# Kernel optimization log

Hardware: AMD Instinct MI355X
Metric: run time of the kernel (lower is better)

Reference implementation:

```python
import jax, jax.numpy as jnp
import numpy as np

T, B, C, HS, RD = 32, 32, 128, 512, 3  # timesteps, batch, state_channels, hidden_size, recurse_depth
HW = 7


def setup_inputs() -> dict:
    key = jax.random.key(0)
    ks = jax.random.split(key, 6)
    x = jax.random.normal(ks[0], (T * B, C, HW, HW), jnp.float32)
    hxs = jax.random.normal(ks[1], (B, 2 * C, HW, HW), jnp.float32)
    masks = jax.random.uniform(ks[2], (T * B,), jnp.float32)
    # ConvLSTMCell: conv over concat(x, h) [2C in] -> 4C gate channels, 3x3, bias
    Wconv = jax.random.normal(ks[3], (4 * C, 2 * C, 3, 3), jnp.float32) * 0.02
    bconv = jnp.zeros((4 * C,), jnp.float32)
    # flat_lin: Linear(C*7*7 -> hidden_size), torch layout [out, in]
    Wlin = jax.random.normal(ks[4], (HS, C * HW * HW), jnp.float32) * 0.02
    blin = jnp.zeros((HS,), jnp.float32)
    return {"x": x, "hxs": hxs, "masks": masks, "Wconv": Wconv, "bconv": bconv, "Wlin": Wlin, "blin": blin}


def reference(x, hxs, masks, Wconv, bconv, Wlin, blin):
    xs = x.reshape(T, B, C, HW, HW)
    ms = masks.reshape(T, B)
    h0, c0 = hxs[:, :C], hxs[:, C:]

    def conv_gates(inp):  # [B, 2C, 7, 7] -> [B, 4C, 7, 7]
        y = jax.lax.conv_general_dilated(
            inp, Wconv, window_strides=(1, 1), padding="SAME",
            dimension_numbers=("NCHW", "OIHW", "NCHW"))
        return y + bconv[None, :, None, None]

    def step(carry, inp):
        h, c = carry
        x_t, m_t = inp
        m = m_t[:, None, None, None]
        h = h * m
        c = c * m
        for _ in range(RD):  # recurse_depth inner unroll (sequential dependency)
            g = conv_gates(jnp.concatenate([x_t, h], axis=1))
            cc_i, cc_f, cc_o, cc_g = jnp.split(g, 4, axis=1)
            i = jax.nn.sigmoid(cc_i)
            f = jax.nn.sigmoid(cc_f)
            o = jax.nn.sigmoid(cc_o)
            gg = jnp.tanh(cc_g)
            c = f * c + i * gg
            h = o * jnp.tanh(c)
        out = jax.nn.relu(c.reshape(B, -1) @ Wlin.T + blin)  # flat_lin applied to c
        return (h, c), out

    (hT, cT), outs = jax.lax.scan(step, (h0, c0), (xs, ms))
    return outs.reshape(T * B, HS), jnp.concatenate([hT, cT], axis=1)
```

## Files before the change

### kernel.cpp

```cpp
#include <hip/hip_runtime.h>
#include <hip/hip_bf16.h>
#include <stdint.h>

#define T_  32
#define B_  32
#define C_  128
#define HS_ 512
#define HW_ 7
#define S_  49
#define CS_  (C_*S_)
#define ICS_ (2*C_*S_)
#define KH_  1152
#define KL_  6272
#define M_   1568
#define N_   512

typedef __attribute__((ext_vector_type(8))) short short8;
typedef __attribute__((ext_vector_type(4))) float f32x4;
typedef __hip_bfloat16 bf16;

union bfbits { bf16 b; short s; };

__device__ __forceinline__ void gl16(const void* g, void* l) {
    __builtin_amdgcn_global_load_lds((const __attribute__((address_space(1))) void*)g,
                                     (__attribute__((address_space(3))) void*)l, 16, 0, 0);
}

__device__ __forceinline__ float sigm_f(float v) { return 1.0f / (1.0f + __expf(-v)); }
__device__ __forceinline__ float tanh_f(float v) { return 1.0f - 2.0f / (__expf(2.0f * v) + 1.0f); }

__global__ __launch_bounds__(256, 2) void k_fgemm(
    const bf16* __restrict__ xTt, const bf16* __restrict__ hT,
    bf16* __restrict__ hTN,
    const bf16* __restrict__ WxP, const bf16* __restrict__ WhP,
    const float* __restrict__ bconv,
    float* __restrict__ Gx, float* __restrict__ cbuf,
    const float* __restrict__ mask_c, const float* __restrict__ mask_a,
    bf16* __restrict__ chist_t, const bf16* __restrict__ zb, int mode0)
{
    __shared__ bf16 sA[2][32 * 64];
    __shared__ bf16 sB[2][64 * 64];
    __shared__ float gld[32][68];

    const int tid = threadIdx.x, lane = tid & 63, w = tid >> 6;
    const int m0 = blockIdx.x * 32, n0 = blockIdx.y * 64;

    const int ar   = tid >> 3;
    const int akq  = tid & 7;
    const int am_  = m0 + ar;
    const int ab   = am_ / S_;
    const int as_  = am_ % S_;
    const int ayy  = as_ / HW_, axx = as_ % HW_;
    const int aswz = ((akq ^ (ar & 7)) << 3);

    const int br0 = tid >> 3;
    const int br1 = (256 + tid) >> 3;
    const int bswz0 = (((tid & 7) ^ (br0 & 7)) << 3);
    const int bswz1 = (((tid & 7) ^ (br1 & 7)) << 3);

    const int NS = mode0 ? 36 : 18;

    f32x4 accX[2], accH[2];
    if (mode0) {
        int np = n0 + w * 16 + (lane & 15);
        float bv = bconv[((np & 3) << 7) + (np >> 2)];
        f32x4 b4 = {bv, bv, bv, bv};
        accX[0] = b4; accX[1] = b4;
        f32x4 z4 = {0.f, 0.f, 0.f, 0.f};
        accH[0] = z4; accH[1] = z4;
    } else {
#pragma unroll
        for (int fm = 0; fm < 2; ++fm) {
            int row = m0 + fm * 16 + ((lane >> 4) << 2);
            int col = n0 + w * 16 + (lane & 15);
#pragma unroll
            for (int j = 0; j < 4; ++j) accH[fm][j] = Gx[(size_t)(row + j) * N_ + col];
        }
    }

    auto stageFor = [&](int st, bf16* lA, bf16* lB) {
        int xphase = (mode0 && st < 18);
        int stl = (mode0 && st >= 18) ? st - 18 : st;
        int kid = stl >> 1, koff = (stl & 1) << 6;
        int ky = kid / 3, kx = kid - ky * 3;
        int y2 = ayy + ky - 1, x2 = axx + kx - 1;
        const bf16* Asrc = xphase ? xTt : hT;
        const bf16* rbase;
        if ((unsigned)y2 < (unsigned)HW_ && (unsigned)x2 < (unsigned)HW_)
            rbase = Asrc + (((size_t)ab * S_ + y2 * HW_ + x2) << 7) + koff;
        else
            rbase = zb;
        gl16(rbase + aswz, lA + w * 512);
        const bf16* Wsrc = xphase ? WxP : WhP;
        gl16(Wsrc + (size_t)(n0 + br0) * KH_ + stl * 64 + bswz0, lB + w * 512);
        gl16(Wsrc + (size_t)(n0 + br1) * KH_ + stl * 64 + bswz1, lB + 2048 + w * 512);
    };

    auto computeFrom = [&](const bf16* sAc, const bf16* sBc, f32x4 (&acc)[2]) {
        short8 af[2][2], bq[2];
#pragma unroll
        for (int kh = 0; kh < 2; ++kh) {
#pragma unroll
            for (int fm = 0; fm < 2; ++fm) {
                int r = fm * 16 + (lane & 15);
                int kc = kh * 4 + (lane >> 4);
                af[fm][kh] = *(const short8*)(sAc + r * 64 + ((kc ^ (r & 7)) << 3));
            }
            { int r = w * 16 + (lane & 15);
              int kc = kh * 4 + (lane >> 4);
              bq[kh] = *(const short8*)(sBc + r * 64 + ((kc ^ (r & 7)) << 3)); }
        }
#pragma unroll
        for (int kh = 0; kh < 2; ++kh)
#pragma unroll
            for (int fm = 0; fm < 2; ++fm)
                acc[fm] = __builtin_amdgcn_mfma_f32_16x16x32_bf16(af[fm][kh], bq[kh], acc[fm], 0, 0, 0);
    };

    stageFor(0, sA[0], sB[0]);
    __syncthreads();

#pragma unroll 1
    for (int st = 0; st < NS; st += 2) {
        if (st + 1 < NS) stageFor(st + 1, sA[1], sB[1]);
        if (mode0 && st < 18) computeFrom(sA[0], sB[0], accX);
        else                  computeFrom(sA[0], sB[0], accH);
        __syncthreads();
        if (st + 2 < NS) stageFor(st + 2, sA[0], sB[0]);
        if (mode0 && st + 1 < 18) computeFrom(sA[1], sB[1], accX);
        else                      computeFrom(sA[1], sB[1], accH);
        __syncthreads();
    }

    if (mode0) {
#pragma unroll
        for (int fm = 0; fm < 2; ++fm) {
            int row = m0 + fm * 16 + ((lane >> 4) << 2);
            int col = n0 + w * 16 + (lane & 15);
#pragma unroll
            for (int j = 0; j < 4; ++j) {
                Gx[(size_t)(row + j) * N_ + col] = accX[fm][j];
                accH[fm][j] += accX[fm][j];
            }
        }
    }

#pragma unroll
    for (int fm = 0; fm < 2; ++fm) {
        int row = fm * 16 + ((lane >> 4) << 2);
        int col = w * 16 + (lane & 15);
#pragma unroll
        for (int j = 0; j < 4; ++j) gld[row + j][col] = accH[fm][j];
    }
    __syncthreads();

#pragma unroll
    for (int q = 0; q < 2; ++q) {
        int e = tid * 2 + q;
        int row = e >> 4, cc = e & 15;
        int m = m0 + row;
        int b = m / S_, s = m % S_;
        int cg = (n0 >> 2) + cc;
        float g0 = gld[row][cc * 4 + 0], g1 = gld[row][cc * 4 + 1];
        float g2 = gld[row][cc * 4 + 2], g3 = gld[row][cc * 4 + 3];
        float ig = sigm_f(g0);
        float fg = sigm_f(g1);
        float og = sigm_f(g2);
        float gg = tanh_f(g3);
        size_t ci = (((size_t)b * S_ + s) << 7) + cg;
        float co = cbuf[ci];
        if (mask_c) co *= mask_c[b];
        float cn = fg * co + ig * gg;
        cbuf[ci] = cn;
        float hn = og * tanh_f(cn);
        float am = mask_a ? mask_a[b] : 1.f;
        hTN[ci] = __float2bfloat16(hn * am);
        if (chist_t) chist_t[(size_t)b * KL_ + s * C_ + cg] = __float2bfloat16(cn);
    }
}

__device__ __forceinline__ void stage64(
    const bf16* __restrict__ srcA, int strideA, int m0, int kA0,
    const bf16* __restrict__ srcB, int strideB, int n0, int kB0,
    bf16* ldsA, bf16* ldsB, int w, int lane)
{
#pragma unroll
    for (int p = 0; p < 2; ++p) {
        int slot = p * 256 + w * 64 + lane;
        int r  = slot >> 3;
        int kq = slot & 7;
        int kqs = (kq ^ (r & 7)) << 3;
        gl16(srcA + (size_t)(m0 + r) * strideA + kA0 + kqs, ldsA + p * 2048 + w * 512);
        gl16(srcB + (size_t)(n0 + r) * strideB + kB0 + kqs, ldsB + p * 2048 + w * 512);
    }
}

__global__ __launch_bounds__(256, 2) void k_lingemm(
    const bf16* __restrict__ Ac, const bf16* __restrict__ Wl,
    const float* __restrict__ blin, float* __restrict__ out)
{
    __shared__ bf16 sA[2][64 * 64];
    __shared__ bf16 sB[2][64 * 64];

    const int tid = threadIdx.x, lane = tid & 63, w = tid >> 6;
    const int wr = w >> 1, wc = w & 1;
    const int m0 = blockIdx.x * 64, n0 = blockIdx.y * 64;

    f32x4 acc[2][2];
#pragma unroll
    for (int fn = 0; fn < 2; ++fn) {
        int np = n0 + wc * 32 + fn * 16 + (lane & 15);
        float bv = blin[np];
        f32x4 b4 = {bv, bv, bv, bv};
        acc[0][fn] = b4; acc[1][fn] = b4;
    }

    auto stageFor = [&](int s2, bf16* lA, bf16* lB) {
        stage64(Ac, KL_, m0, s2 * 64, Wl, KL_, n0, s2 * 64, lA, lB, w, lane);
    };
    auto computeFrom = [&](const bf16* sAc, const bf16* sBc) {
        short8 af[2][2], bq[2][2];
#pragma unroll
        for (int f = 0; f < 2; ++f)
#pragma unroll
            for (int kh = 0; kh < 2; ++kh) {
                { int r = wr * 32 + f * 16 + (lane & 15);
                  int kc = kh * 4 + (lane >> 4);
                  af[f][kh] = *(const short8*)(sAc + r * 64 + ((kc ^ (r & 7)) << 3)); }
                { int r = wc * 32 + f * 16 + (lane & 15);
                  int kc = kh * 4 + (lane >> 4);
                  bq[f][kh] = *(const short8*)(sBc + r * 64 + ((kc ^ (r & 7)) << 3)); }
            }
#pragma unroll
        for (int kh = 0; kh < 2; ++kh)
#pragma unroll
            for (int fm = 0; fm < 2; ++fm)
#pragma unroll
                for (int fn = 0; fn < 2; ++fn)
                    acc[fm][fn] = __builtin_amdgcn_mfma_f32_16x16x32_bf16(
                        af[fm][kh], bq[fn][kh], acc[fm][fn], 0, 0, 0);
    };

    stageFor(0, sA[0], sB[0]);
    __syncthreads();

#pragma unroll 1
    for (int st = 0; st < 98; st += 2) {
        if (st + 1 < 98) stageFor(st + 1, sA[1], sB[1]);
        computeFrom(sA[0], sB[0]);
        __syncthreads();
        if (st + 2 < 98) stageFor(st + 2, sA[0], sB[0]);
        computeFrom(sA[1], sB[1]);
        __syncthreads();
    }

#pragma unroll
    for (int fm = 0; fm < 2; ++fm)
#pragma unroll
        for (int fn = 0; fn < 2; ++fn) {
            int col = n0 + wc * 32 + fn * 16 + (lane & 15);
            int rb  = m0 + wr * 32 + fm * 16 + ((lane >> 4) << 2);
#pragma unroll
            for (int j = 0; j < 4; ++j)
                out[(size_t)(rb + j) * N_ + col] = fmaxf(acc[fm][fn][j], 0.f);
        }
}

__global__ __launch_bounds__(256) void k_wsplit(const float* __restrict__ Wc,
                                               bf16* __restrict__ WxP, bf16* __restrict__ WhP) {
    int idx = blockIdx.x * 256 + threadIdx.x;
    if (idx >= 512 * 288) return;
    int np = idx / 288, kq = idx % 288;
    int oc = ((np & 3) << 7) + (np >> 2);
    int kk = kq * 8;
    int half = kk >= KH_;
    int krel = kk - half * KH_;
    short8 v;
#pragma unroll
    for (int j = 0; j < 8; ++j) {
        int kr = krel + j;
        int kid = kr >> 7, ic = (kr & 127) + half * 128;
        bfbits bb; bb.b = __float2bfloat16(Wc[((size_t)oc * 256 + ic) * 9 + kid]);
        v[j] = bb.s;
    }
    bf16* dst = half ? WhP : WxP;
    *reinterpret_cast<short8*>(dst + (size_t)np * KH_ + krel) = v;
}

__global__ __launch_bounds__(256) void k_wlin2(const float* __restrict__ Wl, bf16* __restrict__ Wp) {
    int idx = blockIdx.x * 256 + threadIdx.x;
    if (idx >= 512 * 784) return;
    int np = idx / 784, kq = idx % 784;
    short8 v;
#pragma unroll
    for (int j = 0; j < 8; ++j) {
        int kp = kq * 8 + j;
        int s = kp >> 7, c = kp & 127;
        bfbits bb; bb.b = __float2bfloat16(Wl[(size_t)np * KL_ + c * S_ + s]);
        v[j] = bb.s;
    }
    *reinterpret_cast<short8*>(Wp + (size_t)np * KL_ + kq * 8) = v;
}

__global__ __launch_bounds__(256) void k_xpose(const float* __restrict__ x, bf16* __restrict__ xT) {
    int idx = blockIdx.x * 256 + threadIdx.x;
    if (idx >= 1024 * 784) return;
    int r = idx / 784;
    int rem = idx % 784;
    int s = rem / 16, c8 = (rem & 15) * 8;
    const float* sp = x + (size_t)r * CS_ + c8 * S_ + s;
    short8 v;
#pragma unroll
    for (int j = 0; j < 8; ++j) { bfbits bb; bb.b = __float2bfloat16(sp[j * S_]); v[j] = bb.s; }
    *reinterpret_cast<short8*>(xT + (((size_t)r * S_ + s) << 7) + c8) = v;
}

__global__ __launch_bounds__(256) void k_hcprep(const float* __restrict__ hxs,
                                                const float* __restrict__ mask0,
                                                bf16* __restrict__ hT, float* __restrict__ cbuf) {
    int idx = blockIdx.x * 256 + threadIdx.x;
    if (idx >= 32 * 784) return;
    int b = idx / 784;
    int rem = idx % 784;
    int s = rem / 16, c8 = (rem & 15) * 8;
    float m = mask0[b];
    const float* hp = hxs + (size_t)b * ICS_ + c8 * S_ + s;
    const float* cp = hp + CS_;
    size_t o = (((size_t)b * S_ + s) << 7) + c8;
    short8 v;
#pragma unroll
    for (int j = 0; j < 8; ++j) {
        bfbits bb; bb.b = __float2bfloat16(hp[j * S_] * m); v[j] = bb.s;
        cbuf[o + j] = cp[j * S_];
    }
    *reinterpret_cast<short8*>(hT + o) = v;
}

__global__ __launch_bounds__(256) void k_zero16(uint4* __restrict__ p, int n) {
    int i = blockIdx.x * 256 + threadIdx.x;
    if (i < n) p[i] = make_uint4(0, 0, 0, 0);
}

__global__ __launch_bounds__(256) void k_final(const bf16* __restrict__ hT, const float* __restrict__ cbuf,
                                               float* __restrict__ out) {
    int i = blockIdx.x * 256 + threadIdx.x;
    if (i >= B_ * ICS_) return;
    int b = i / ICS_, r = i % ICS_;
    int ch = r / S_, s = r % S_;
    size_t o = (((size_t)b * S_ + s) << 7);
    out[i] = (ch < C_) ? __bfloat162float(hT[o + ch]) : cbuf[o + (ch - C_)];
}

extern "C" void kernel_launch(void* const* d_in, const int* in_sizes, int n_in,
                              void* d_out, int out_size, void* d_ws, size_t ws_size,
                              hipStream_t stream) {
    (void)in_sizes; (void)n_in; (void)out_size; (void)ws_size;
    const float* x     = (const float*)d_in[0];
    const float* hxs   = (const float*)d_in[1];
    const float* masks = (const float*)d_in[2];
    const float* Wconv = (const float*)d_in[3];
    const float* bconv = (const float*)d_in[4];
    const float* Wlin  = (const float*)d_in[5];
    const float* blin  = (const float*)d_in[6];
    float* out = (float*)d_out;

    uint8_t* p = (uint8_t*)d_ws;
    bf16* WxP   = (bf16*)p;   p += (size_t)512 * KH_ * 2;
    bf16* WhP   = (bf16*)p;   p += (size_t)512 * KH_ * 2;
    bf16* Wlp   = (bf16*)p;   p += (size_t)512 * KL_ * 2;
    bf16* xT    = (bf16*)p;   p += (size_t)1024 * S_ * C_ * 2;
    bf16* hA    = (bf16*)p;   p += (size_t)B_ * S_ * C_ * 2;
    bf16* hB    = (bf16*)p;   p += (size_t)B_ * S_ * C_ * 2;
    float* cbuf = (float*)p;  p += (size_t)B_ * S_ * C_ * 4;
    float* Gx   = (float*)p;  p += (size_t)M_ * N_ * 4;
    bf16* chist = (bf16*)p;   p += (size_t)1024 * KL_ * 2;
    bf16* zb    = (bf16*)p;   p += 1024;
    bf16* hbufs[2] = {hA, hB};

    k_wsplit<<<576, 256, 0, stream>>>(Wconv, WxP, WhP);
    k_wlin2<<<1568, 256, 0, stream>>>(Wlin, Wlp);
    k_xpose<<<3136, 256, 0, stream>>>(x, xT);
    k_hcprep<<<98, 256, 0, stream>>>(hxs, masks, hA, cbuf);
    k_zero16<<<1, 256, 0, stream>>>((uint4*)zb, 64);

    int g = 0;
    for (int t = 0; t < T_; ++t) {
        const bf16* xTt = xT + (size_t)t * B_ * S_ * C_;
        for (int rd = 0; rd < 3; ++rd) {
            const float* mc = (rd == 0) ? masks + (size_t)t * B_ : nullptr;
            const float* ma = (rd == 2 && t < T_ - 1) ? masks + (size_t)(t + 1) * B_ : nullptr;
            bf16* ct = (rd == 2) ? chist + (size_t)t * B_ * KL_ : nullptr;
            k_fgemm<<<dim3(49, 8), 256, 0, stream>>>(
                (rd == 0) ? xTt : nullptr, hbufs[g & 1], hbufs[(g + 1) & 1],
                WxP, WhP, bconv, Gx, cbuf, mc, ma, ct, zb, (rd == 0) ? 1 : 0);
            ++g;
        }
    }

    k_lingemm<<<dim3(16, 8), 256, 0, stream>>>(chist, Wlp, blin, out);
    k_final<<<1568, 256, 0, stream>>>(hbufs[0], cbuf, out + (size_t)T_ * B_ * HS_);
}
```

Before: 1.714 ms.

## Enlarge recurrent conv GEMM tile to 64x64 with K=128 stages

The per-step conv-gate GEMM now uses 64x64 output tiles per block (2x2 warp layout) instead of 32x64, and both GEMMs stage 128-wide K chunks per step with a single sync per stage instead of 64-wide chunks. The aim is to halve the number of barriers and global-to-LDS staging rounds and to raise operand reuse per loaded tile. In exchange the recurrent kernel launches only 200 blocks instead of 392, which lowers parallelism across the GPU's compute units on this latency-bound sequential chain. The LDS footprint grows to 64KB, and Gx is padded so the partial last row tile stays in bounds.

```diff
diff --git a/kernel.cpp b/kernel.cpp
--- a/kernel.cpp
+++ b/kernel.cpp
@@ -13,6 +13,7 @@
 #define KH_  1152
 #define KL_  6272
 #define M_   1568
+#define MR_  1600
 #define N_   512
 
 typedef __attribute__((ext_vector_type(8))) short short8;
@@ -38,128 +39,145 @@
     const float* __restrict__ mask_c, const float* __restrict__ mask_a,
     bf16* __restrict__ chist_t, const bf16* __restrict__ zb, int mode0)
 {
-    __shared__ bf16 sA[2][32 * 64];
-    __shared__ bf16 sB[2][64 * 64];
-    __shared__ float gld[32][68];
+    __shared__ __align__(16) uint8_t smem[65536];
+    bf16* sA = (bf16*)smem;
+    bf16* sB = (bf16*)(smem + 32768);
+    float (*gld)[68] = (float(*)[68])smem;
 
     const int tid = threadIdx.x, lane = tid & 63, w = tid >> 6;
-    const int m0 = blockIdx.x * 32, n0 = blockIdx.y * 64;
-
-    const int ar   = tid >> 3;
-    const int akq  = tid & 7;
-    const int am_  = m0 + ar;
-    const int ab   = am_ / S_;
-    const int as_  = am_ % S_;
-    const int ayy  = as_ / HW_, axx = as_ % HW_;
-    const int aswz = ((akq ^ (ar & 7)) << 3);
-
-    const int br0 = tid >> 3;
-    const int br1 = (256 + tid) >> 3;
-    const int bswz0 = (((tid & 7) ^ (br0 & 7)) << 3);
-    const int bswz1 = (((tid & 7) ^ (br1 & 7)) << 3);
-
-    const int NS = mode0 ? 36 : 18;
-
-    f32x4 accX[2], accH[2];
+    const int wr = w >> 1, wc = w & 1;
+    const int m0 = blockIdx.x * 64, n0 = blockIdx.y * 64;
+
+    const int kq = tid & 15, rr = tid >> 4;
+    const int swz = ((kq ^ rr) << 3);
+    int abS[4], ay[4], ax[4]; bool rok[4];
+#pragma unroll
+    for (int q = 0; q < 4; ++q) {
+        int ra = m0 + q * 16 + rr;
+        rok[q] = ra < M_;
+        int b = ra / S_, s = ra - b * S_;
+        abS[q] = b * S_;
+        ay[q] = s / HW_; ax[q] = s - ay[q] * HW_;
+    }
+
+    const int NS = mode0 ? 18 : 9;
+
+    f32x4 accX[2][2], accH[2][2];
     if (mode0) {
-        int np = n0 + w * 16 + (lane & 15);
-        float bv = bconv[((np & 3) << 7) + (np >> 2)];
-        f32x4 b4 = {bv, bv, bv, bv};
-        accX[0] = b4; accX[1] = b4;
-        f32x4 z4 = {0.f, 0.f, 0.f, 0.f};
-        accH[0] = z4; accH[1] = z4;
+#pragma unroll
+        for (int fn = 0; fn < 2; ++fn) {
+            int np = n0 + wc * 32 + fn * 16 + (lane & 15);
+            float bv = bconv[((np & 3) << 7) + (np >> 2)];
+            f32x4 b4 = {bv, bv, bv, bv};
+            accX[0][fn] = b4; accX[1][fn] = b4;
+            f32x4 z4 = {0.f, 0.f, 0.f, 0.f};
+            accH[0][fn] = z4; accH[1][fn] = z4;
+        }
     } else {
 #pragma unroll
         for (int fm = 0; fm < 2; ++fm) {
-            int row = m0 + fm * 16 + ((lane >> 4) << 2);
-            int col = n0 + w * 16 + (lane & 15);
-#pragma unroll
-            for (int j = 0; j < 4; ++j) accH[fm][j] = Gx[(size_t)(row + j) * N_ + col];
-        }
-    }
-
-    auto stageFor = [&](int st, bf16* lA, bf16* lB) {
-        int xphase = (mode0 && st < 18);
-        int stl = (mode0 && st >= 18) ? st - 18 : st;
-        int kid = stl >> 1, koff = (stl & 1) << 6;
+            int row = m0 + wr * 32 + fm * 16 + ((lane >> 4) << 2);
+#pragma unroll
+            for (int fn = 0; fn < 2; ++fn) {
+                int col = n0 + wc * 32 + fn * 16 + (lane & 15);
+#pragma unroll
+                for (int j = 0; j < 4; ++j)
+                    accH[fm][fn][j] = Gx[(size_t)(row + j) * N_ + col];
+            }
+        }
+    }
+
+    auto stage = [&](int st, int dbuf) {
+        int xph = (mode0 && st < 9);
+        int kid = xph ? st : (mode0 ? st - 9 : st);
         int ky = kid / 3, kx = kid - ky * 3;
-        int y2 = ayy + ky - 1, x2 = axx + kx - 1;
-        const bf16* Asrc = xphase ? xTt : hT;
-        const bf16* rbase;
-        if ((unsigned)y2 < (unsigned)HW_ && (unsigned)x2 < (unsigned)HW_)
-            rbase = Asrc + (((size_t)ab * S_ + y2 * HW_ + x2) << 7) + koff;
-        else
-            rbase = zb;
-        gl16(rbase + aswz, lA + w * 512);
-        const bf16* Wsrc = xphase ? WxP : WhP;
-        gl16(Wsrc + (size_t)(n0 + br0) * KH_ + stl * 64 + bswz0, lB + w * 512);
-        gl16(Wsrc + (size_t)(n0 + br1) * KH_ + stl * 64 + bswz1, lB + 2048 + w * 512);
+        const bf16* Asrc = xph ? xTt : hT;
+        const bf16* Wsrc = xph ? WxP : WhP;
+        bf16* lA = sA + dbuf * 8192;
+        bf16* lB = sB + dbuf * 8192;
+#pragma unroll
+        for (int q = 0; q < 4; ++q) {
+            int y2 = ay[q] + ky - 1, x2 = ax[q] + kx - 1;
+            const bf16* rb = (rok[q] && (unsigned)y2 < (unsigned)HW_ && (unsigned)x2 < (unsigned)HW_)
+                ? Asrc + (((size_t)(abS[q] + y2 * HW_ + x2)) << 7) : zb;
+            gl16(rb + swz, lA + q * 2048 + w * 512);
+            gl16(Wsrc + (size_t)(n0 + q * 16 + rr) * KH_ + kid * 128 + swz, lB + q * 2048 + w * 512);
+        }
     };
 
-    auto computeFrom = [&](const bf16* sAc, const bf16* sBc, f32x4 (&acc)[2]) {
-        short8 af[2][2], bq[2];
-#pragma unroll
-        for (int kh = 0; kh < 2; ++kh) {
+    auto compute = [&](int dbuf, f32x4 (&acc)[2][2]) {
+        const bf16* lA = sA + dbuf * 8192;
+        const bf16* lB = sB + dbuf * 8192;
+        short8 af[2][4], bq[2][4];
+#pragma unroll
+        for (int kh = 0; kh < 4; ++kh) {
+            int c = kh * 4 + (lane >> 4);
+            int xr = (c ^ (lane & 15)) << 3;
 #pragma unroll
             for (int fm = 0; fm < 2; ++fm) {
-                int r = fm * 16 + (lane & 15);
-                int kc = kh * 4 + (lane >> 4);
-                af[fm][kh] = *(const short8*)(sAc + r * 64 + ((kc ^ (r & 7)) << 3));
-            }
-            { int r = w * 16 + (lane & 15);
-              int kc = kh * 4 + (lane >> 4);
-              bq[kh] = *(const short8*)(sBc + r * 64 + ((kc ^ (r & 7)) << 3)); }
-        }
-#pragma unroll
-        for (int kh = 0; kh < 2; ++kh)
+                int r = wr * 32 + fm * 16 + (lane & 15);
+                af[fm][kh] = *(const short8*)(lA + r * 128 + xr);
+            }
+#pragma unroll
+            for (int fn = 0; fn < 2; ++fn) {
+                int r = wc * 32 + fn * 16 + (lane & 15);
+                bq[fn][kh] = *(const short8*)(lB + r * 128 + xr);
+            }
+        }
+#pragma unroll
+        for (int kh = 0; kh < 4; ++kh)
 #pragma unroll
             for (int fm = 0; fm < 2; ++fm)
-                acc[fm] = __builtin_amdgcn_mfma_f32_16x16x32_bf16(af[fm][kh], bq[kh], acc[fm], 0, 0, 0);
+#pragma unroll
+                for (int fn = 0; fn < 2; ++fn)
+                    acc[fm][fn] = __builtin_amdgcn_mfma_f32_16x16x32_bf16(
+                        af[fm][kh], bq[fn][kh], acc[fm][fn], 0, 0, 0);
     };
 
-    stageFor(0, sA[0], sB[0]);
+    stage(0, 0);
     __syncthreads();
-
 #pragma unroll 1
-    for (int st = 0; st < NS; st += 2) {
-        if (st + 1 < NS) stageFor(st + 1, sA[1], sB[1]);
-        if (mode0 && st < 18) computeFrom(sA[0], sB[0], accX);
-        else                  computeFrom(sA[0], sB[0], accH);
+    for (int st = 0; st < NS; ++st) {
+        if (st + 1 < NS) stage(st + 1, (st + 1) & 1);
+        if (mode0 && st < 9) compute(st & 1, accX);
+        else                 compute(st & 1, accH);
         __syncthreads();
-        if (st + 2 < NS) stageFor(st + 2, sA[0], sB[0]);
-        if (mode0 && st + 1 < 18) computeFrom(sA[1], sB[1], accX);
-        else                      computeFrom(sA[1], sB[1], accH);
-        __syncthreads();
     }
 
     if (mode0) {
 #pragma unroll
         for (int fm = 0; fm < 2; ++fm) {
-            int row = m0 + fm * 16 + ((lane >> 4) << 2);
-            int col = n0 + w * 16 + (lane & 15);
-#pragma unroll
-            for (int j = 0; j < 4; ++j) {
-                Gx[(size_t)(row + j) * N_ + col] = accX[fm][j];
-                accH[fm][j] += accX[fm][j];
-            }
-        }
-    }
-
-#pragma unroll
-    for (int fm = 0; fm < 2; ++fm) {
-        int row = fm * 16 + ((lane >> 4) << 2);
-        int col = w * 16 + (lane & 15);
-#pragma unroll
-        for (int j = 0; j < 4; ++j) gld[row + j][col] = accH[fm][j];
-    }
+            int row = m0 + wr * 32 + fm * 16 + ((lane >> 4) << 2);
+#pragma unroll
+            for (int fn = 0; fn < 2; ++fn) {
+                int col = n0 + wc * 32 + fn * 16 + (lane & 15);
+#pragma unroll
+                for (int j = 0; j < 4; ++j) {
+                    Gx[(size_t)(row + j) * N_ + col] = accX[fm][fn][j];
+                    accH[fm][fn][j] += accX[fm][fn][j];
+                }
+            }
+        }
+    }
+
+#pragma unroll
+    for (int fm = 0; fm < 2; ++fm)
+#pragma unroll
+        for (int fn = 0; fn < 2; ++fn) {
+            int row = wr * 32 + fm * 16 + ((lane >> 4) << 2);
+            int col = wc * 32 + fn * 16 + (lane & 15);
+#pragma unroll
+            for (int j = 0; j < 4; ++j) gld[row + j][col] = accH[fm][fn][j];
+        }
     __syncthreads();
 
 #pragma unroll
-    for (int q = 0; q < 2; ++q) {
-        int e = tid * 2 + q;
+    for (int q2 = 0; q2 < 4; ++q2) {
+        int e = tid + q2 * 256;
         int row = e >> 4, cc = e & 15;
         int m = m0 + row;
-        int b = m / S_, s = m % S_;
+        if (m >= M_) continue;
+        int b = m / S_, s = m - b * S_;
         int cg = (n0 >> 2) + cc;
         float g0 = gld[row][cc * 4 + 0], g1 = gld[row][cc * 4 + 1];
         float g2 = gld[row][cc * 4 + 2], g3 = gld[row][cc * 4 + 3];
@@ -179,32 +197,19 @@
     }
 }
 
-__device__ __forceinline__ void stage64(
-    const bf16* __restrict__ srcA, int strideA, int m0, int kA0,
-    const bf16* __restrict__ srcB, int strideB, int n0, int kB0,
-    bf16* ldsA, bf16* ldsB, int w, int lane)
-{
-#pragma unroll
-    for (int p = 0; p < 2; ++p) {
-        int slot = p * 256 + w * 64 + lane;
-        int r  = slot >> 3;
-        int kq = slot & 7;
-        int kqs = (kq ^ (r & 7)) << 3;
-        gl16(srcA + (size_t)(m0 + r) * strideA + kA0 + kqs, ldsA + p * 2048 + w * 512);
-        gl16(srcB + (size_t)(n0 + r) * strideB + kB0 + kqs, ldsB + p * 2048 + w * 512);
-    }
-}
-
 __global__ __launch_bounds__(256, 2) void k_lingemm(
     const bf16* __restrict__ Ac, const bf16* __restrict__ Wl,
     const float* __restrict__ blin, float* __restrict__ out)
 {
-    __shared__ bf16 sA[2][64 * 64];
-    __shared__ bf16 sB[2][64 * 64];
+    __shared__ __align__(16) uint8_t smem[65536];
+    bf16* sA = (bf16*)smem;
+    bf16* sB = (bf16*)(smem + 32768);
 
     const int tid = threadIdx.x, lane = tid & 63, w = tid >> 6;
     const int wr = w >> 1, wc = w & 1;
     const int m0 = blockIdx.x * 64, n0 = blockIdx.y * 64;
+    const int kq = tid & 15, rr = tid >> 4;
+    const int swz = ((kq ^ rr) << 3);
 
     f32x4 acc[2][2];
 #pragma unroll
@@ -215,24 +220,36 @@
         acc[0][fn] = b4; acc[1][fn] = b4;
     }
 
-    auto stageFor = [&](int s2, bf16* lA, bf16* lB) {
-        stage64(Ac, KL_, m0, s2 * 64, Wl, KL_, n0, s2 * 64, lA, lB, w, lane);
+    auto stage = [&](int st, int dbuf) {
+        bf16* lA = sA + dbuf * 8192;
+        bf16* lB = sB + dbuf * 8192;
+#pragma unroll
+        for (int q = 0; q < 4; ++q) {
+            gl16(Ac + (size_t)(m0 + q * 16 + rr) * KL_ + st * 128 + swz, lA + q * 2048 + w * 512);
+            gl16(Wl + (size_t)(n0 + q * 16 + rr) * KL_ + st * 128 + swz, lB + q * 2048 + w * 512);
+        }
     };
-    auto computeFrom = [&](const bf16* sAc, const bf16* sBc) {
-        short8 af[2][2], bq[2][2];
-#pragma unroll
-        for (int f = 0; f < 2; ++f)
-#pragma unroll
-            for (int kh = 0; kh < 2; ++kh) {
-                { int r = wr * 32 + f * 16 + (lane & 15);
-                  int kc = kh * 4 + (lane >> 4);
-                  af[f][kh] = *(const short8*)(sAc + r * 64 + ((kc ^ (r & 7)) << 3)); }
-                { int r = wc * 32 + f * 16 + (lane & 15);
-                  int kc = kh * 4 + (lane >> 4);
-                  bq[f][kh] = *(const short8*)(sBc + r * 64 + ((kc ^ (r & 7)) << 3)); }
-            }
-#pragma unroll
-        for (int kh = 0; kh < 2; ++kh)
+    auto compute = [&](int dbuf) {
+        const bf16* lA = sA + dbuf * 8192;
+        const bf16* lB = sB + dbuf * 8192;
+        short8 af[2][4], bq[2][4];
+#pragma unroll
+        for (int kh = 0; kh < 4; ++kh) {
+            int c = kh * 4 + (lane >> 4);
+            int xr = (c ^ (lane & 15)) << 3;
+#pragma unroll
+            for (int fm = 0; fm < 2; ++fm) {
+                int r = wr * 32 + fm * 16 + (lane & 15);
+                af[fm][kh] = *(const short8*)(lA + r * 128 + xr);
+            }
+#pragma unroll
+            for (int fn = 0; fn < 2; ++fn) {
+                int r = wc * 32 + fn * 16 + (lane & 15);
+                bq[fn][kh] = *(const short8*)(lB + r * 128 + xr);
+            }
+        }
+#pragma unroll
+        for (int kh = 0; kh < 4; ++kh)
 #pragma unroll
             for (int fm = 0; fm < 2; ++fm)
 #pragma unroll
@@ -241,16 +258,12 @@
                         af[fm][kh], bq[fn][kh], acc[fm][fn], 0, 0, 0);
     };
 
-    stageFor(0, sA[0], sB[0]);
+    stage(0, 0);
     __syncthreads();
-
 #pragma unroll 1
-    for (int st = 0; st < 98; st += 2) {
-        if (st + 1 < 98) stageFor(st + 1, sA[1], sB[1]);
-        computeFrom(sA[0], sB[0]);
-        __syncthreads();
-        if (st + 2 < 98) stageFor(st + 2, sA[0], sB[0]);
-        computeFrom(sA[1], sB[1]);
+    for (int st = 0; st < 49; ++st) {
+        if (st + 1 < 49) stage(st + 1, (st + 1) & 1);
+        compute(st & 1);
         __syncthreads();
     }
 
@@ -372,7 +385,7 @@
     bf16* hA    = (bf16*)p;   p += (size_t)B_ * S_ * C_ * 2;
     bf16* hB    = (bf16*)p;   p += (size_t)B_ * S_ * C_ * 2;
     float* cbuf = (float*)p;  p += (size_t)B_ * S_ * C_ * 4;
-    float* Gx   = (float*)p;  p += (size_t)M_ * N_ * 4;
+    float* Gx   = (float*)p;  p += (size_t)MR_ * N_ * 4;
     bf16* chist = (bf16*)p;   p += (size_t)1024 * KL_ * 2;
     bf16* zb    = (bf16*)p;   p += 1024;
     bf16* hbufs[2] = {hA, hB};
@@ -390,7 +403,7 @@
             const float* mc = (rd == 0) ? masks + (size_t)t * B_ : nullptr;
             const float* ma = (rd == 2 && t < T_ - 1) ? masks + (size_t)(t + 1) * B_ : nullptr;
             bf16* ct = (rd == 2) ? chist + (size_t)t * B_ * KL_ : nullptr;
-            k_fgemm<<<dim3(49, 8), 256, 0, stream>>>(
+            k_fgemm<<<dim3(25, 8), 256, 0, stream>>>(
                 (rd == 0) ? xTt : nullptr, hbufs[g & 1], hbufs[(g + 1) & 1],
                 WxP, WhP, bconv, Gx, cbuf, mc, ma, ct, zb, (rd == 0) ? 1 : 0);
             ++g;
```

After: 1.403 ms. -18.1%, faster.
